# Optimization experiments

Measured on AMD Instinct MI355X. Metric: run time of the kernel, lower is better.

The kernel has to match this reference:

```python
import jax, jax.numpy as jnp
import numpy as np

H, DK, DV = 16, 64, 64  # head_nums, key_size, head_size
D_MODEL = H * DK        # 1024
OUT_DIM = H * DV        # 1024


def setup_inputs() -> dict:
    key = jax.random.key(0)
    ks = jax.random.split(key, 12)
    B, S = 2, 2048
    scale = 0.02
    return {
        "q": jax.random.normal(ks[0], (B, S, D_MODEL), jnp.float32),
        "k": jax.random.normal(ks[1], (B, S, D_MODEL), jnp.float32),
        "v": jax.random.normal(ks[2], (B, S, D_MODEL), jnp.float32),
        "Wq": jax.random.normal(ks[3], (D_MODEL, H * DK), jnp.float32) * scale,
        "bq": jnp.zeros((H * DK,), jnp.float32),
        "Wk": jax.random.normal(ks[4], (D_MODEL, H * DK), jnp.float32) * scale,
        "bk": jnp.zeros((H * DK,), jnp.float32),
        "Wv": jax.random.normal(ks[5], (D_MODEL, OUT_DIM), jnp.float32) * scale,
        "bv": jnp.zeros((OUT_DIM,), jnp.float32),
        "Wo": jax.random.normal(ks[6], (OUT_DIM, OUT_DIM), jnp.float32) * scale,
        "bo": jnp.zeros((OUT_DIM,), jnp.float32),
    }


def reference(q, k, v, Wq, bq, Wk, bk, Wv, bv, Wo, bo):
    B, S, _ = q.shape
    # linear projections, split heads
    qw = (q @ Wq + bq).reshape(B, S, H, DK)   # [B,S,H,dk]
    kw = (k @ Wk + bk).reshape(B, S, H, DK)   # [B,S,H,dk]
    vw = (v @ Wv + bv).reshape(B, S, H, DV)   # [B,S,H,dv]
    # scaled dot-product attention scores
    att = jnp.einsum("bshk,bqhk->bhsq", qw, kw) / (DK ** 0.5)  # [B,H,S,S]
    att = jax.nn.softmax(att, axis=-1)
    out = jnp.einsum("bhsq,bqhk->bhsk", att, vw)  # [B,H,S,dv]
    out = out.transpose(0, 2, 1, 3).reshape(B, S, OUT_DIM)  # merge heads
    return out @ Wo + bo
```

## Files before the change

kernel.cpp:

```cpp
#include <hip/hip_runtime.h>
#include <hip/hip_bf16.h>

#define BB 2
#define SS 2048
#define HH 16
#define DD 64
#define DM 1024
#define MM (BB*SS)

typedef __attribute__((ext_vector_type(4))) float f32x4;
typedef __attribute__((ext_vector_type(16))) float f32x16;
typedef __attribute__((ext_vector_type(8))) short s16x8;
typedef __attribute__((ext_vector_type(2))) int i32x2;

__device__ __forceinline__ unsigned short f2bf(float f){
  unsigned int u = __float_as_uint(f);
  u += 0x7FFF + ((u >> 16) & 1);
  return (unsigned short)(u >> 16);
}

__device__ __forceinline__ f32x4 zero4(){ f32x4 z = {0.f,0.f,0.f,0.f}; return z; }

__device__ __forceinline__ unsigned int cvtpk(float a, float b){
  unsigned int r;
  asm("v_cvt_pk_bf16_f32 %0, %1, %2" : "=v"(r) : "v"(a), "v"(b));
  return r;
}

__device__ __forceinline__ void gload_lds16(const void* g, void* l){
  __builtin_amdgcn_global_load_lds(
    (const __attribute__((address_space(1))) unsigned int*)g,
    (__attribute__((address_space(3))) unsigned int*)l, 16, 0, 0);
}

__global__ __launch_bounds__(256) void wtrans_kernel(
    const float* __restrict__ Wq, const float* __restrict__ Wk,
    const float* __restrict__ Wv, const float* __restrict__ Wo,
    short* __restrict__ wt){
  __shared__ float tile[64][65];
  const float* src = (blockIdx.y==0)?Wq:(blockIdx.y==1)?Wk:(blockIdx.y==2)?Wv:Wo;
  short* dst = wt + (size_t)blockIdx.y * ((size_t)DM*DM);
  int tk = (blockIdx.x >> 4) * 64;
  int tn = (blockIdx.x & 15) * 64;
  int t = threadIdx.x;
  int r = t >> 2;
  int c4 = (t & 3) << 4;
  const float* p = src + (size_t)(tk + r) * DM + tn + c4;
  #pragma unroll
  for (int i = 0; i < 4; ++i){
    float4 vv = *(const float4*)(p + i*4);
    tile[r][c4 + i*4 + 0] = vv.x;
    tile[r][c4 + i*4 + 1] = vv.y;
    tile[r][c4 + i*4 + 2] = vv.z;
    tile[r][c4 + i*4 + 3] = vv.w;
  }
  __syncthreads();
  s16x8 o0, o1;
  #pragma unroll
  for (int j = 0; j < 8; ++j) o0[j] = (short)f2bf(tile[c4 + j][r]);
  #pragma unroll
  for (int j = 0; j < 8; ++j) o1[j] = (short)f2bf(tile[c4 + 8 + j][r]);
  short* qd = dst + (size_t)(tn + r) * DM + tk + c4;
  *(s16x8*)qd       = o0;
  *(s16x8*)(qd + 8) = o1;
}

#define GEMM_PRE_COMMON() \
  int m0 = blockIdx.x * 128, n0 = blockIdx.y * 64; \
  int t = threadIdx.x; \
  int w = t >> 6, lane = t & 63, g = lane >> 4, c = lane & 15; \
  int wm = (w >> 1) * 64, wn = (w & 1) * 32; \
  f32x4 acc[4][2]; \
  _Pragma("unroll") for (int i=0;i<4;++i) \
    _Pragma("unroll") for (int j=0;j<2;++j) acc[i][j] = zero4(); \
  int srow = t >> 3; \
  int scol = ((t & 7) ^ (srow & 7)) * 8; \
  const short* Bp = BT + (size_t)(n0 + srow) * DM + scol; \
  int rsw = (c & 7) << 4; \
  int adst = srow*128 + (t & 7)*16;

#define BSTAGE(k0_, BB_) { \
  gload_lds16(Bp + (k0_),          (char*)(BB_) + w*1024); \
  gload_lds16(Bp + 32*DM + (k0_),  (char*)(BB_) + 4096 + w*1024); \
}

#define ALOAD_F32(k0_) { \
  _Pragma("unroll") for (int ch=0; ch<4; ++ch){ \
    areg[2*ch]   = *(const float4*)(Apf + (size_t)ch*32*DM + (k0_)); \
    areg[2*ch+1] = *(const float4*)(Apf + (size_t)ch*32*DM + (k0_) + 4); \
  } }

#define AWRITE(AB_) { \
  _Pragma("unroll") for (int ch=0; ch<4; ++ch){ \
    int4 pk4; \
    pk4.x = (int)cvtpk(areg[2*ch].x,   areg[2*ch].y); \
    pk4.y = (int)cvtpk(areg[2*ch].z,   areg[2*ch].w); \
    pk4.z = (int)cvtpk(areg[2*ch+1].x, areg[2*ch+1].y); \
    pk4.w = (int)cvtpk(areg[2*ch+1].z, areg[2*ch+1].w); \
    *(int4*)((char*)(AB_) + ch*4096 + adst) = pk4; \
  } }

#define ASTAGE_BF16(k0_, AB_) { \
  gload_lds16(Apb + (k0_),          (char*)(AB_) + w*1024); \
  gload_lds16(Apb + 32*DM + (k0_),  (char*)(AB_) + 4096  + w*1024); \
  gload_lds16(Apb + 64*DM + (k0_),  (char*)(AB_) + 8192  + w*1024); \
  gload_lds16(Apb + 96*DM + (k0_),  (char*)(AB_) + 12288 + w*1024); \
}

#define GCOMP(AB_, BB_) { \
  s16x8 af[4][2], bfr[2][2]; \
  _Pragma("unroll") for (int mi=0;mi<4;++mi){ \
    const char* arow = (const char*)(AB_) + (wm + mi*16 + c)*128; \
    af[mi][0] = *(const s16x8*)(arow + ((g*16) ^ rsw)); \
    af[mi][1] = *(const s16x8*)(arow + ((64 + g*16) ^ rsw)); \
  } \
  _Pragma("unroll") for (int ni=0;ni<2;++ni){ \
    const char* brow = (const char*)(BB_) + (wn + ni*16 + c)*128; \
    bfr[ni][0] = *(const s16x8*)(brow + ((g*16) ^ rsw)); \
    bfr[ni][1] = *(const s16x8*)(brow + ((64 + g*16) ^ rsw)); \
  } \
  _Pragma("unroll") for (int mi=0;mi<4;++mi) \
    _Pragma("unroll") for (int ni=0;ni<2;++ni){ \
      acc[mi][ni] = __builtin_amdgcn_mfma_f32_16x16x32_bf16(af[mi][0], bfr[ni][0], acc[mi][ni], 0,0,0); \
      acc[mi][ni] = __builtin_amdgcn_mfma_f32_16x16x32_bf16(af[mi][1], bfr[ni][1], acc[mi][ni], 0,0,0); \
    } \
}

#define GEMM_LOOP_F32() \
  float4 areg[8]; \
  ALOAD_F32(0) \
  BSTAGE(0, &Bs[0][0]) \
  AWRITE(&As[0][0]) \
  __syncthreads(); \
  for (int kk = 0; kk < DM; kk += 128){ \
    if (kk + 64 < DM){ ALOAD_F32(kk+64) BSTAGE(kk+64, &Bs[1][0]) } \
    GCOMP(&As[0][0], &Bs[0][0]) \
    if (kk + 64 < DM){ AWRITE(&As[1][0]) } \
    __syncthreads(); \
    if (kk + 128 < DM){ ALOAD_F32(kk+128) BSTAGE(kk+128, &Bs[0][0]) } \
    GCOMP(&As[1][0], &Bs[1][0]) \
    if (kk + 128 < DM){ AWRITE(&As[0][0]) } \
    __syncthreads(); \
  }

#define GEMM_LOOP_BF16() \
  ASTAGE_BF16(0, &As[0][0]) \
  BSTAGE(0, &Bs[0][0]) \
  __syncthreads(); \
  for (int kk = 0; kk < DM; kk += 128){ \
    if (kk + 64 < DM){ ASTAGE_BF16(kk+64, &As[1][0]) BSTAGE(kk+64, &Bs[1][0]) } \
    GCOMP(&As[0][0], &Bs[0][0]) \
    __syncthreads(); \
    if (kk + 128 < DM){ ASTAGE_BF16(kk+128, &As[0][0]) BSTAGE(kk+128, &Bs[0][0]) } \
    GCOMP(&As[1][0], &Bs[1][0]) \
    __syncthreads(); \
  }

__global__ __launch_bounds__(256) void gemm_qkv3_kernel(
    const float* __restrict__ qs, const float* __restrict__ ks,
    const float* __restrict__ vs, const short* __restrict__ WT3,
    const float* __restrict__ bq, const float* __restrict__ bk,
    const float* __restrict__ bv,
    short* __restrict__ Qh, short* __restrict__ Kh, short* __restrict__ Vt,
    float qscale){
  __shared__ __align__(16) short As[2][128*64];
  __shared__ __align__(16) short Bs[2][64*64];
  int z = blockIdx.z;
  const float* A    = (z==0) ? qs : (z==1) ? ks : vs;
  const short* BT   = WT3 + (size_t)z * ((size_t)DM*DM);
  const float* bias = (z==0) ? bq : (z==1) ? bk : bv;
  GEMM_PRE_COMMON()
  const float* Apf = A + (size_t)(m0 + srow) * DM + scol;
  GEMM_LOOP_F32()
  if (z < 2){
    short* outh = (z==0) ? Qh : Kh;
    float scale = (z==0) ? qscale : 1.0f;
    #pragma unroll
    for (int ni=0;ni<2;++ni){
      int col = n0 + wn + ni*16 + c;
      float bvv = bias[col];
      int hh = col >> 6, d = col & 63;
      #pragma unroll
      for (int mi=0;mi<4;++mi){
        #pragma unroll
        for (int r=0;r<4;++r){
          int row = m0 + wm + mi*16 + g*4 + r;
          int b = row >> 11, s = row & (SS-1);
          float val = (acc[mi][ni][r] + bvv) * scale;
          outh[((((size_t)b*HH + hh)*SS + s) << 6) + d] = (short)f2bf(val);
        }
      }
    }
  } else {
    #pragma unroll
    for (int ni=0;ni<2;++ni){
      int col = n0 + wn + ni*16 + c;
      float bvv = bias[col];
      int hh = col >> 6, d = col & 63;
      #pragma unroll
      for (int mi=0;mi<4;++mi){
        int row = m0 + wm + mi*16 + g*4;
        int b = row >> 11, s = row & (SS-1);
        i32x2 pk2;
        pk2.x = (int)cvtpk(acc[mi][ni][0] + bvv, acc[mi][ni][1] + bvv);
        pk2.y = (int)cvtpk(acc[mi][ni][2] + bvv, acc[mi][ni][3] + bvv);
        *(i32x2*)(Vt + (((size_t)(b*HH + hh)*64 + d) * SS + s)) = pk2;
      }
    }
  }
}

__global__ __launch_bounds__(256) void gemm_out_kernel(
    const short* __restrict__ A, const short* __restrict__ BT,
    const float* __restrict__ bias, float* __restrict__ out){
  __shared__ __align__(16) short As[2][128*64];
  __shared__ __align__(16) short Bs[2][64*64];
  GEMM_PRE_COMMON()
  const short* Apb = A + (size_t)(m0 + srow) * DM + scol;
  GEMM_LOOP_BF16()
  #pragma unroll
  for (int ni=0;ni<2;++ni){
    int col = n0 + wn + ni*16 + c;
    float bvv = bias[col];
    #pragma unroll
    for (int mi=0;mi<4;++mi){
      #pragma unroll
      for (int r=0;r<4;++r){
        int row = m0 + wm + mi*16 + g*4 + r;
        out[(size_t)row * DM + col] = acc[mi][ni][r] + bvv;
      }
    }
  }
}

__global__ __launch_bounds__(256) void attn_kernel(
    const short* __restrict__ Qh, const short* __restrict__ Kh,
    const short* __restrict__ Vt, short* __restrict__ Oh){
  __shared__ __align__(16) short SMEM[16384];
  int bh = blockIdx.y;
  int qb = blockIdx.x * 128;
  int t = threadIdx.x, w = t >> 6, lane = t & 63;
  int lq = lane & 31, h = lane >> 5;
  int qrow0 = qb + w*32;

  const short* qg = Qh + (((size_t)bh*SS + qrow0 + lq) << 6) + h*8;
  s16x8 qf[4];
  #pragma unroll
  for (int kc=0;kc<4;++kc) qf[kc] = *(const s16x8*)(qg + kc*16);

  f32x16 z16;
  #pragma unroll
  for (int i=0;i<16;++i) z16[i] = 0.f;
  f32x16 oA, oB;
  #pragma unroll
  for (int i=0;i<16;++i){ oA[i]=0.f; oB[i]=0.f; }
  float l = 0.f;
  const char* kbase = (const char*)(Kh + (((size_t)bh*SS) << 6));
  const char* vbase = (const char*)(Vt + ((size_t)bh*64) * SS);

  int rsel = lane >> 3;
  int csw  = ((lane & 7) << 4) ^ (rsel << 4);
  int swr  = (lane & 7) << 4;

  const char* smem = (const char*)&SMEM[0];
  const char* kr0 = smem + lq*128 + (( 0 + h*16) ^ swr);
  const char* kr1 = smem + lq*128 + ((32 + h*16) ^ swr);
  const char* kr2 = smem + lq*128 + ((64 + h*16) ^ swr);
  const char* kr3 = smem + lq*128 + ((96 + h*16) ^ swr);
  char* smem_w = (char*)&SMEM[0] + w*2048;

#define STAGE_K(T, BOFF) { \
    const char* kg = kbase + (((size_t)((T)*64 + w*16 + rsel)) << 7) + csw; \
    gload_lds16(kg,        smem_w + (BOFF)); \
    gload_lds16(kg + 1024, smem_w + (BOFF) + 1024); \
  }
#define STAGE_V(T, BOFF) { \
    const char* vg = vbase + (size_t)(w*16 + rsel) * (SS*2) + ((size_t)(T) << 7) + csw; \
    gload_lds16(vg,            smem_w + 16384 + (BOFF)); \
    gload_lds16(vg + 8*(SS*2), smem_w + 16384 + (BOFF) + 1024); \
  }

#define MFMA32(a_, b_, c_) __builtin_amdgcn_mfma_f32_32x32x16_bf16(a_, b_, c_, 0,0,0)

#define QK_PART(KOFF, sAn, sBn) { \
    s16x8 kf; \
    __builtin_amdgcn_s_setprio(1); \
    kf = *(const s16x8*)(kr0 + (KOFF));        sAn = MFMA32(kf, qf[0], z16); \
    kf = *(const s16x8*)(kr0 + (KOFF) + 4096); sBn = MFMA32(kf, qf[0], z16); \
    kf = *(const s16x8*)(kr1 + (KOFF));        sAn = MFMA32(kf, qf[1], sAn); \
    kf = *(const s16x8*)(kr1 + (KOFF) + 4096); sBn = MFMA32(kf, qf[1], sBn); \
    kf = *(const s16x8*)(kr2 + (KOFF));        sAn = MFMA32(kf, qf[2], sAn); \
    kf = *(const s16x8*)(kr2 + (KOFF) + 4096); sBn = MFMA32(kf, qf[2], sBn); \
    kf = *(const s16x8*)(kr3 + (KOFF));        sAn = MFMA32(kf, qf[3], sAn); \
    kf = *(const s16x8*)(kr3 + (KOFF) + 4096); sBn = MFMA32(kf, qf[3], sBn); \
    __builtin_amdgcn_s_setprio(0); \
  }

#define SMPV_PART(VOFF, sAp, sBp) { \
    float lp = 0.f; \
    unsigned int cA[8], cB[8]; \
    _Pragma("unroll") \
    for (int i=0;i<8;++i){ \
      float a0 = __builtin_amdgcn_exp2f(sAp[2*i]); \
      float a1 = __builtin_amdgcn_exp2f(sAp[2*i+1]); \
      float b0 = __builtin_amdgcn_exp2f(sBp[2*i]); \
      float b1 = __builtin_amdgcn_exp2f(sBp[2*i+1]); \
      lp += (a0 + a1) + (b0 + b1); \
      cA[i] = cvtpk(a0, a1); \
      cB[i] = cvtpk(b0, b1); \
    } \
    l += lp; \
    asm("v_permlane32_swap_b32 %0, %1" : "+v"(cA[0]), "+v"(cA[2])); \
    asm("v_permlane32_swap_b32 %0, %1" : "+v"(cA[1]), "+v"(cA[3])); \
    asm("v_permlane32_swap_b32 %0, %1" : "+v"(cA[4]), "+v"(cA[6])); \
    asm("v_permlane32_swap_b32 %0, %1" : "+v"(cA[5]), "+v"(cA[7])); \
    asm("v_permlane32_swap_b32 %0, %1" : "+v"(cB[0]), "+v"(cB[2])); \
    asm("v_permlane32_swap_b32 %0, %1" : "+v"(cB[1]), "+v"(cB[3])); \
    asm("v_permlane32_swap_b32 %0, %1" : "+v"(cB[4]), "+v"(cB[6])); \
    asm("v_permlane32_swap_b32 %0, %1" : "+v"(cB[5]), "+v"(cB[7])); \
    s16x8 pbf0, pbf1, pbf2, pbf3; \
    { unsigned int* p0 = (unsigned int*)&pbf0; \
      p0[0]=cA[0]; p0[1]=cA[1]; p0[2]=cA[2]; p0[3]=cA[3]; \
      unsigned int* p1 = (unsigned int*)&pbf1; \
      p1[0]=cA[4]; p1[1]=cA[5]; p1[2]=cA[6]; p1[3]=cA[7]; \
      unsigned int* p2 = (unsigned int*)&pbf2; \
      p2[0]=cB[0]; p2[1]=cB[1]; p2[2]=cB[2]; p2[3]=cB[3]; \
      unsigned int* p3 = (unsigned int*)&pbf3; \
      p3[0]=cB[4]; p3[1]=cB[5]; p3[2]=cB[6]; p3[3]=cB[7]; } \
    s16x8 vf; \
    __builtin_amdgcn_s_setprio(1); \
    vf = *(const s16x8*)(kr0 + 16384 + (VOFF));        oA = MFMA32(vf, pbf0, oA); \
    vf = *(const s16x8*)(kr0 + 16384 + (VOFF) + 4096); oB = MFMA32(vf, pbf0, oB); \
    vf = *(const s16x8*)(kr1 + 16384 + (VOFF));        oA = MFMA32(vf, pbf1, oA); \
    vf = *(const s16x8*)(kr1 + 16384 + (VOFF) + 4096); oB = MFMA32(vf, pbf1, oB); \
    vf = *(const s16x8*)(kr2 + 16384 + (VOFF));        oA = MFMA32(vf, pbf2, oA); \
    vf = *(const s16x8*)(kr2 + 16384 + (VOFF) + 4096); oB = MFMA32(vf, pbf2, oB); \
    vf = *(const s16x8*)(kr3 + 16384 + (VOFF));        oA = MFMA32(vf, pbf3, oA); \
    vf = *(const s16x8*)(kr3 + 16384 + (VOFF) + 4096); oB = MFMA32(vf, pbf3, oB); \
    __builtin_amdgcn_s_setprio(0); \
  }

  f32x16 sA0, sB0, sA1, sB1;

  STAGE_K(0, 0)
  __syncthreads();
  STAGE_K(1, 8192)
  STAGE_V(0, 0)
  QK_PART(0, sA0, sB0)

  for (int i = 1; i <= 29; i += 2){
    __syncthreads();
    STAGE_K(i+1, 0)
    STAGE_V(i, 8192)
    QK_PART(8192, sA1, sB1)
    SMPV_PART(0, sA0, sB0)
    __syncthreads();
    STAGE_K(i+2, 8192)
    STAGE_V(i+1, 0)
    QK_PART(0, sA0, sB0)
    SMPV_PART(8192, sA1, sB1)
  }
  __syncthreads();
  STAGE_V(31, 8192)
  QK_PART(8192, sA1, sB1)
  SMPV_PART(0, sA0, sB0)
  __syncthreads();
  SMPV_PART(8192, sA1, sB1)

#undef STAGE_K
#undef STAGE_V
#undef QK_PART
#undef SMPV_PART

  l += __shfl_xor(l, 32);
  float inv = 1.f / l;
  int b = bh >> 4, hh = bh & 15;
  short* ob = Oh + (((size_t)(b*SS + qrow0 + lq)) << 10) + hh*64 + 4*h;
  #pragma unroll
  for (int rg=0;rg<4;++rg){
    i32x2 pk;
    pk.x = (int)cvtpk(oA[rg*4+0]*inv, oA[rg*4+1]*inv);
    pk.y = (int)cvtpk(oA[rg*4+2]*inv, oA[rg*4+3]*inv);
    *(i32x2*)(ob + 8*rg) = pk;
    pk.x = (int)cvtpk(oB[rg*4+0]*inv, oB[rg*4+1]*inv);
    pk.y = (int)cvtpk(oB[rg*4+2]*inv, oB[rg*4+3]*inv);
    *(i32x2*)(ob + 32 + 8*rg) = pk;
  }
}

extern "C" void kernel_launch(void* const* d_in, const int* in_sizes, int n_in,
                              void* d_out, int out_size, void* d_ws, size_t ws_size,
                              hipStream_t stream){
  const float* q  = (const float*)d_in[0];
  const float* k  = (const float*)d_in[1];
  const float* v  = (const float*)d_in[2];
  const float* Wq = (const float*)d_in[3];
  const float* bq = (const float*)d_in[4];
  const float* Wk = (const float*)d_in[5];
  const float* bk = (const float*)d_in[6];
  const float* Wv = (const float*)d_in[7];
  const float* bv = (const float*)d_in[8];
  const float* Wo = (const float*)d_in[9];
  const float* bo = (const float*)d_in[10];
  (void)in_sizes; (void)n_in; (void)out_size; (void)ws_size;

  short* wsp = (short*)d_ws;
  const size_t MW = 1048576;
  short* WT3 = wsp;
  short* WTo = wsp + 3*MW;
  short* Qh  = wsp + 4*MW;
  short* Kh  = wsp + 8*MW;
  short* Oh  = wsp + 12*MW;
  short* Vt  = wsp + 16*MW;

  const float QSCALE = 0.125f * 1.44269504088896f;
  wtrans_kernel<<<dim3(256,4), 256, 0, stream>>>(Wq, Wk, Wv, Wo, wsp);
  gemm_qkv3_kernel<<<dim3(32,16,3), 256, 0, stream>>>(q, k, v, WT3, bq, bk, bv,
                                                      Qh, Kh, Vt, QSCALE);
  attn_kernel<<<dim3(16,32), 256, 0, stream>>>(Qh, Kh, Vt, Oh);
  gemm_out_kernel<<<dim3(32,16), 256, 0, stream>>>(Oh, WTo, bo, (float*)d_out);
}
```

Baseline: 122.2 us.

## Halve GEMM K-tile to 32 with new LDS swizzle, remap attention block order

The projection and output GEMMs now stage K-slices of 32 instead of 64 per buffer. This halves LDS usage and the number of register-held A values, and the loop runs twice as many iterations with a new XOR swizzle for the narrower rows. The goal is higher occupancy and fewer registers, paid for with more barriers per unit of work. The attention kernel also remaps block indices so that consecutive blocks cover 8 different heads with the same query block, to change L2 locality.

```diff
diff --git a/kernel.cpp b/kernel.cpp
--- a/kernel.cpp
+++ b/kernel.cpp
@@ -65,6 +65,7 @@
   *(s16x8*)(qd + 8) = o1;
 }
 
+
 #define GEMM_PRE_COMMON() \
   int m0 = blockIdx.x * 128, n0 = blockIdx.y * 64; \
   int t = threadIdx.x; \
@@ -73,73 +74,63 @@
   f32x4 acc[4][2]; \
   _Pragma("unroll") for (int i=0;i<4;++i) \
     _Pragma("unroll") for (int j=0;j<2;++j) acc[i][j] = zero4(); \
-  int srow = t >> 3; \
-  int scol = ((t & 7) ^ (srow & 7)) * 8; \
-  const short* Bp = BT + (size_t)(n0 + srow) * DM + scol; \
-  int rsw = (c & 7) << 4; \
-  int adst = srow*128 + (t & 7)*16;
-
-#define BSTAGE(k0_, BB_) { \
-  gload_lds16(Bp + (k0_),          (char*)(BB_) + w*1024); \
-  gload_lds16(Bp + 32*DM + (k0_),  (char*)(BB_) + 4096 + w*1024); \
-}
+  int csl = ((lane & 3) ^ (lane >> 4)) * 8; \
+  const short* Bp = BT + (size_t)(n0 + w*16 + (lane >> 2)) * DM + csl; \
+  int rofs = (g ^ (c >> 2)) << 4;
+
+#define BSTAGE(k0_, BB_) gload_lds16(Bp + (k0_), (char*)(BB_) + w*1024);
 
 #define ALOAD_F32(k0_) { \
-  _Pragma("unroll") for (int ch=0; ch<4; ++ch){ \
-    areg[2*ch]   = *(const float4*)(Apf + (size_t)ch*32*DM + (k0_)); \
-    areg[2*ch+1] = *(const float4*)(Apf + (size_t)ch*32*DM + (k0_) + 4); \
-  } }
+  areg[0] = *(const float4*)(Apf + (k0_)); \
+  areg[1] = *(const float4*)(Apf + (k0_) + 4); \
+  areg[2] = *(const float4*)(Apf + (k0_) + 8); \
+  areg[3] = *(const float4*)(Apf + (k0_) + 12); \
+}
 
 #define AWRITE(AB_) { \
-  _Pragma("unroll") for (int ch=0; ch<4; ++ch){ \
-    int4 pk4; \
-    pk4.x = (int)cvtpk(areg[2*ch].x,   areg[2*ch].y); \
-    pk4.y = (int)cvtpk(areg[2*ch].z,   areg[2*ch].w); \
-    pk4.z = (int)cvtpk(areg[2*ch+1].x, areg[2*ch+1].y); \
-    pk4.w = (int)cvtpk(areg[2*ch+1].z, areg[2*ch+1].w); \
-    *(int4*)((char*)(AB_) + ch*4096 + adst) = pk4; \
-  } }
+  int4 p0, p1; \
+  p0.x = (int)cvtpk(areg[0].x, areg[0].y); \
+  p0.y = (int)cvtpk(areg[0].z, areg[0].w); \
+  p0.z = (int)cvtpk(areg[1].x, areg[1].y); \
+  p0.w = (int)cvtpk(areg[1].z, areg[1].w); \
+  p1.x = (int)cvtpk(areg[2].x, areg[2].y); \
+  p1.y = (int)cvtpk(areg[2].z, areg[2].w); \
+  p1.z = (int)cvtpk(areg[3].x, areg[3].y); \
+  p1.w = (int)cvtpk(areg[3].z, areg[3].w); \
+  *(int4*)((char*)(AB_) + ad0) = p0; \
+  *(int4*)((char*)(AB_) + ad1) = p1; \
+}
 
 #define ASTAGE_BF16(k0_, AB_) { \
-  gload_lds16(Apb + (k0_),          (char*)(AB_) + w*1024); \
-  gload_lds16(Apb + 32*DM + (k0_),  (char*)(AB_) + 4096  + w*1024); \
-  gload_lds16(Apb + 64*DM + (k0_),  (char*)(AB_) + 8192  + w*1024); \
-  gload_lds16(Apb + 96*DM + (k0_),  (char*)(AB_) + 12288 + w*1024); \
+  gload_lds16(Apb + (k0_),         (char*)(AB_) + w*2048); \
+  gload_lds16(Apb + 16*DM + (k0_), (char*)(AB_) + w*2048 + 1024); \
 }
 
 #define GCOMP(AB_, BB_) { \
-  s16x8 af[4][2], bfr[2][2]; \
-  _Pragma("unroll") for (int mi=0;mi<4;++mi){ \
-    const char* arow = (const char*)(AB_) + (wm + mi*16 + c)*128; \
-    af[mi][0] = *(const s16x8*)(arow + ((g*16) ^ rsw)); \
-    af[mi][1] = *(const s16x8*)(arow + ((64 + g*16) ^ rsw)); \
-  } \
-  _Pragma("unroll") for (int ni=0;ni<2;++ni){ \
-    const char* brow = (const char*)(BB_) + (wn + ni*16 + c)*128; \
-    bfr[ni][0] = *(const s16x8*)(brow + ((g*16) ^ rsw)); \
-    bfr[ni][1] = *(const s16x8*)(brow + ((64 + g*16) ^ rsw)); \
-  } \
+  s16x8 af[4], bfr[2]; \
   _Pragma("unroll") for (int mi=0;mi<4;++mi) \
-    _Pragma("unroll") for (int ni=0;ni<2;++ni){ \
-      acc[mi][ni] = __builtin_amdgcn_mfma_f32_16x16x32_bf16(af[mi][0], bfr[ni][0], acc[mi][ni], 0,0,0); \
-      acc[mi][ni] = __builtin_amdgcn_mfma_f32_16x16x32_bf16(af[mi][1], bfr[ni][1], acc[mi][ni], 0,0,0); \
-    } \
+    af[mi] = *(const s16x8*)((const char*)(AB_) + (wm + mi*16 + c)*64 + rofs); \
+  _Pragma("unroll") for (int ni=0;ni<2;++ni) \
+    bfr[ni] = *(const s16x8*)((const char*)(BB_) + (wn + ni*16 + c)*64 + rofs); \
+  _Pragma("unroll") for (int mi=0;mi<4;++mi) \
+    _Pragma("unroll") for (int ni=0;ni<2;++ni) \
+      acc[mi][ni] = __builtin_amdgcn_mfma_f32_16x16x32_bf16(af[mi], bfr[ni], acc[mi][ni], 0,0,0); \
 }
 
 #define GEMM_LOOP_F32() \
-  float4 areg[8]; \
+  float4 areg[4]; \
   ALOAD_F32(0) \
   BSTAGE(0, &Bs[0][0]) \
   AWRITE(&As[0][0]) \
   __syncthreads(); \
-  for (int kk = 0; kk < DM; kk += 128){ \
-    if (kk + 64 < DM){ ALOAD_F32(kk+64) BSTAGE(kk+64, &Bs[1][0]) } \
+  for (int kk = 0; kk < DM; kk += 64){ \
+    if (kk + 32 < DM){ ALOAD_F32(kk+32) BSTAGE(kk+32, &Bs[1][0]) } \
     GCOMP(&As[0][0], &Bs[0][0]) \
-    if (kk + 64 < DM){ AWRITE(&As[1][0]) } \
+    if (kk + 32 < DM){ AWRITE(&As[1][0]) } \
     __syncthreads(); \
-    if (kk + 128 < DM){ ALOAD_F32(kk+128) BSTAGE(kk+128, &Bs[0][0]) } \
+    if (kk + 64 < DM){ ALOAD_F32(kk+64) BSTAGE(kk+64, &Bs[0][0]) } \
     GCOMP(&As[1][0], &Bs[1][0]) \
-    if (kk + 128 < DM){ AWRITE(&As[0][0]) } \
+    if (kk + 64 < DM){ AWRITE(&As[0][0]) } \
     __syncthreads(); \
   }
 
@@ -147,11 +138,11 @@
   ASTAGE_BF16(0, &As[0][0]) \
   BSTAGE(0, &Bs[0][0]) \
   __syncthreads(); \
-  for (int kk = 0; kk < DM; kk += 128){ \
-    if (kk + 64 < DM){ ASTAGE_BF16(kk+64, &As[1][0]) BSTAGE(kk+64, &Bs[1][0]) } \
+  for (int kk = 0; kk < DM; kk += 64){ \
+    if (kk + 32 < DM){ ASTAGE_BF16(kk+32, &As[1][0]) BSTAGE(kk+32, &Bs[1][0]) } \
     GCOMP(&As[0][0], &Bs[0][0]) \
     __syncthreads(); \
-    if (kk + 128 < DM){ ASTAGE_BF16(kk+128, &As[0][0]) BSTAGE(kk+128, &Bs[0][0]) } \
+    if (kk + 64 < DM){ ASTAGE_BF16(kk+64, &As[0][0]) BSTAGE(kk+64, &Bs[0][0]) } \
     GCOMP(&As[1][0], &Bs[1][0]) \
     __syncthreads(); \
   }
@@ -163,14 +154,18 @@
     const float* __restrict__ bv,
     short* __restrict__ Qh, short* __restrict__ Kh, short* __restrict__ Vt,
     float qscale){
-  __shared__ __align__(16) short As[2][128*64];
-  __shared__ __align__(16) short Bs[2][64*64];
+  __shared__ __align__(16) short As[2][128*32];
+  __shared__ __align__(16) short Bs[2][64*32];
   int z = blockIdx.z;
   const float* A    = (z==0) ? qs : (z==1) ? ks : vs;
   const short* BT   = WT3 + (size_t)z * ((size_t)DM*DM);
   const float* bias = (z==0) ? bq : (z==1) ? bk : bv;
   GEMM_PRE_COMMON()
-  const float* Apf = A + (size_t)(m0 + srow) * DM + scol;
+  const float* Apf = A + (size_t)(m0 + (t >> 1)) * DM + (t & 1) * 16;
+  int s_ = (t >> 3) & 3;
+  int j0 = (t & 1) * 2;
+  int ad0 = (t >> 1)*64 + ((j0 ^ s_) << 4);
+  int ad1 = (t >> 1)*64 + (((j0 + 1) ^ s_) << 4);
   GEMM_LOOP_F32()
   if (z < 2){
     short* outh = (z==0) ? Qh : Kh;
@@ -213,10 +208,10 @@
 __global__ __launch_bounds__(256) void gemm_out_kernel(
     const short* __restrict__ A, const short* __restrict__ BT,
     const float* __restrict__ bias, float* __restrict__ out){
-  __shared__ __align__(16) short As[2][128*64];
-  __shared__ __align__(16) short Bs[2][64*64];
+  __shared__ __align__(16) short As[2][128*32];
+  __shared__ __align__(16) short Bs[2][64*32];
   GEMM_PRE_COMMON()
-  const short* Apb = A + (size_t)(m0 + srow) * DM + scol;
+  const short* Apb = A + (size_t)(m0 + w*32 + (lane >> 2)) * DM + csl;
   GEMM_LOOP_BF16()
   #pragma unroll
   for (int ni=0;ni<2;++ni){
@@ -237,8 +232,9 @@
     const short* __restrict__ Qh, const short* __restrict__ Kh,
     const short* __restrict__ Vt, short* __restrict__ Oh){
   __shared__ __align__(16) short SMEM[16384];
-  int bh = blockIdx.y;
-  int qb = blockIdx.x * 128;
+  int n = blockIdx.x + (blockIdx.y << 4);
+  int bh = (n & 7) | ((n >> 7) << 3);
+  int qb = ((n >> 3) & 15) * 128;
   int t = threadIdx.x, w = t >> 6, lane = t & 63;
   int lq = lane & 31, h = lane >> 5;
   int qrow0 = qb + w*32;
```

Result: slower. 139.9 us (+14.5%).
